# Kernel optimization log

Measured on AMD Instinct MI355X. Metric: run time of the kernel, lower is better.

The kernel has to match this reference:

```python
import jax, jax.numpy as jnp
import numpy as np

N_QUBITS = 4
N_LAYERS = 3
INV_SQRT2 = 0.7071067811865476
BSZ = 262144


def _apply_ry(state, wire, theta):
    # state: [B,2,2,2,2] complex; theta: [B] (per-batch rotation angle)
    s = jnp.moveaxis(state, wire + 1, -1)
    a0, a1 = s[..., 0], s[..., 1]
    c = jnp.cos(theta * 0.5)[:, None, None, None]
    sn = jnp.sin(theta * 0.5)[:, None, None, None]
    out = jnp.stack([c * a0 - sn * a1, sn * a0 + c * a1], axis=-1)
    return jnp.moveaxis(out, -1, wire + 1)


def _apply_h(state, wire):
    s = jnp.moveaxis(state, wire + 1, -1)
    a0, a1 = s[..., 0], s[..., 1]
    out = jnp.stack([(a0 + a1) * INV_SQRT2, (a0 - a1) * INV_SQRT2], axis=-1)
    return jnp.moveaxis(out, -1, wire + 1)


def _apply_crz(state, cw, tw, phi):
    # controlled-RZ: phase exp(-/+ i*phi/2) on |c=1,t=0/1>; phi is a scalar param
    s = jnp.moveaxis(state, (cw + 1, tw + 1), (-2, -1))
    phase = jnp.exp(1j * phi * jnp.array([-0.5, 0.5], dtype=jnp.float32)).astype(s.dtype)
    s = s.at[..., 1, :].multiply(phase)
    return jnp.moveaxis(s, (-2, -1), (cw + 1, tw + 1))


def _circuit(angles, weights):
    # angles: [B,4]; weights: [12]; returns PauliZ expvals [B,4]
    B = angles.shape[0]
    state = jnp.zeros((B, 2, 2, 2, 2), jnp.complex64).at[:, 0, 0, 0, 0].set(1.0)
    for i in range(N_QUBITS):
        state = _apply_ry(state, i, angles[:, i])
    for l in range(N_LAYERS):
        lp = weights[N_QUBITS * l: N_QUBITS * (l + 1)]
        for i in range(N_QUBITS):
            state = _apply_crz(state, i, (i + 1) % N_QUBITS, lp[i])
        for i in range(N_QUBITS):
            state = _apply_h(state, i)
    p = state.real ** 2 + state.imag ** 2  # [B,2,2,2,2] probabilities
    z = jnp.stack(
        [jnp.take(p, 0, axis=w + 1).sum(axis=(1, 2, 3))
         - jnp.take(p, 1, axis=w + 1).sum(axis=(1, 2, 3))
         for w in range(N_QUBITS)],
        axis=-1,
    )
    return z


def setup_inputs() -> dict:
    key = jax.random.key(0)
    k1, k2, k3, k4 = jax.random.split(key, 4)
    x = jax.random.uniform(k1, (BSZ, 16), dtype=jnp.float32)
    weights = jax.random.normal(k2, (N_LAYERS * N_QUBITS,), dtype=jnp.float32)
    lin_w = jax.random.normal(k3, (2, 16), dtype=jnp.float32) * 0.25
    lin_b = jax.random.normal(k4, (2,), dtype=jnp.float32) * 0.1
    return {"x": x, "weights": weights, "lin_w": lin_w, "lin_b": lin_b}


def reference(x, weights, lin_w, lin_b):
    bsz = x.shape[0]
    # 4x4 image -> four 2x2 patches in loop order (0,0),(0,2),(2,0),(2,2);
    # each patch flattened row-major: [x[j,k], x[j,k+1], x[j+1,k], x[j+1,k+1]]
    xv = x.reshape(bsz, 2, 2, 2, 2).transpose(0, 1, 3, 2, 4).reshape(bsz * 4, 4)
    q = _circuit(xv, weights).reshape(bsz, 16)  # patch-major feature order as in torch cat
    logits = q @ lin_w.T + lin_b
    return jax.nn.softmax(logits, axis=1)
```

## Files before the change

### kernel.cpp

```cpp
#include <hip/hip_runtime.h>


__device__ __forceinline__ float layer_angle(const float* __restrict__ w,
                                             int l, int idx) {
    float ang = 0.f;
    #pragma unroll
    for (int g = 0; g < 4; ++g) {
        int cb = (idx >> (3 - g)) & 1;
        int tb = (idx >> (3 - ((g + 1) & 3))) & 1;
        if (cb) ang += (tb ? 0.5f : -0.5f) * w[l * 4 + g];
    }
    return ang;
}

__global__ __launch_bounds__(256) void precompute_tensors(
    const float* __restrict__ weights,
    const float* __restrict__ lin_w,
    const float* __restrict__ lin_b,
    float* __restrict__ ws)
{
    __shared__ float2 U1[256], U2[256], U[256];
    __shared__ float zeta[4][16];
    __shared__ float G[4][256];
    __shared__ float A[4][3][64];
    __shared__ float B[4][9][16];
    __shared__ float C1[4][27][4];
    int t = threadIdx.x;
    int i = t >> 4, j = t & 15;

    {
        float sgn = (__popc(i & j) & 1) ? -1.f : 1.f;
        float a = layer_angle(weights, 0, j);
        U1[t] = make_float2(sgn * __cosf(a), sgn * __sinf(a));
    }
    if (t < 64) {
        int s = t >> 4, k = t & 15;
        float z = 0.f;
        #pragma unroll
        for (int w = 0; w < 4; ++w) {
            float sg = ((k >> (3 - w)) & 1) ? -1.f : 1.f;
            z += (lin_w[s * 4 + w] - lin_w[16 + s * 4 + w]) * sg;
        }
        zeta[s][k] = z;
    }
    __syncthreads();
    {
        float ar = 0.f, ai = 0.f;
        for (int k = 0; k < 16; ++k) {
            float sgn = (__popc(i & k) & 1) ? -1.f : 1.f;
            float a = layer_angle(weights, 1, k);
            float cr = sgn * __cosf(a), ci = sgn * __sinf(a);
            float2 u = U1[k * 16 + j];
            ar += cr * u.x - ci * u.y;
            ai += cr * u.y + ci * u.x;
        }
        U2[t] = make_float2(ar, ai);
    }
    __syncthreads();
    {
        float ar = 0.f, ai = 0.f;
        for (int k = 0; k < 16; ++k) {
            float sgn = (__popc(i & k) & 1) ? -1.f : 1.f;
            float a = layer_angle(weights, 2, k);
            float cr = sgn * __cosf(a), ci = sgn * __sinf(a);
            float2 u = U2[k * 16 + j];
            ar += cr * u.x - ci * u.y;
            ai += cr * u.y + ci * u.x;
        }
        U[t] = make_float2(ar, ai);
    }
    __syncthreads();
    {
        float g[4] = {0, 0, 0, 0};
        for (int k = 0; k < 16; ++k) {
            float2 uki = U[k * 16 + i], ukj = U[k * 16 + j];
            float p = uki.x * ukj.x + uki.y * ukj.y;
            #pragma unroll
            for (int s = 0; s < 4; ++s) g[s] += zeta[s][k] * p;
        }
        #pragma unroll
        for (int s = 0; s < 4; ++s) G[s][t] = g[s];
    }
    __syncthreads();
    for (int e = t; e < 768; e += 256) {
        int m = e / 192, r = e % 192;
        int t3 = r / 64, q = r % 64;
        int ih = q >> 3, jh = q & 7;
        float g00 = G[m][(ih * 2 + 0) * 16 + jh * 2 + 0];
        float g01 = G[m][(ih * 2 + 0) * 16 + jh * 2 + 1];
        float g10 = G[m][(ih * 2 + 1) * 16 + jh * 2 + 0];
        float g11 = G[m][(ih * 2 + 1) * 16 + jh * 2 + 1];
        A[m][t3][q] = (t3 == 0) ? g00 + g11 : (t3 == 1) ? g00 - g11 : g01 + g10;
    }
    __syncthreads();
    for (int e = t; e < 576; e += 256) {
        int m = e / 144, r = e % 144;
        int t2 = r / 48; r %= 48;
        int t3 = r / 16, q = r % 16;
        int ih = q >> 2, jh = q & 3;
        float a00 = A[m][t3][(ih * 2 + 0) * 8 + jh * 2 + 0];
        float a01 = A[m][t3][(ih * 2 + 0) * 8 + jh * 2 + 1];
        float a10 = A[m][t3][(ih * 2 + 1) * 8 + jh * 2 + 0];
        float a11 = A[m][t3][(ih * 2 + 1) * 8 + jh * 2 + 1];
        B[m][t2 * 3 + t3][q] = (t2 == 0) ? a00 + a11
                             : (t2 == 1) ? a00 - a11 : a01 + a10;
    }
    __syncthreads();
    for (int e = t; e < 432; e += 256) {
        int m = e / 108, r = e % 108;
        int t1 = r / 36; r %= 36;
        int t23 = r / 4, q = r % 4;
        int ih = q >> 1, jh = q & 1;
        float b00 = B[m][t23][(ih * 2 + 0) * 4 + jh * 2 + 0];
        float b01 = B[m][t23][(ih * 2 + 0) * 4 + jh * 2 + 1];
        float b10 = B[m][t23][(ih * 2 + 1) * 4 + jh * 2 + 0];
        float b11 = B[m][t23][(ih * 2 + 1) * 4 + jh * 2 + 1];
        C1[m][t1 * 9 + t23][q] = (t1 == 0) ? b00 + b11
                               : (t1 == 1) ? b00 - b11 : b01 + b10;
    }
    __syncthreads();
    {
        const float scale = 1.f / 65536.f;
        float bias = lin_b[0] - lin_b[1];
        for (int e = t; e < 324; e += 256) {
            int m = e / 81, r = e % 81;
            int t0 = r / 27, t123 = r % 27;
            const float* c = C1[m][t123];
            float v = (t0 == 0) ? c[0] + c[3] : (t0 == 1) ? c[0] - c[3]
                                              : c[1] + c[2];
            float val = v * scale;
            if (e == 0) val += bias;
            int t1 = t123 / 9, k = t123 % 9;
            ws[(m * 9 + t0 * 3 + t1) * 12 + k] = val;
        }
    }
}

__global__ __launch_bounds__(256) void qcircuit_kernel(
    const float* __restrict__ x,
    const float* __restrict__ tab,
    float* __restrict__ out,
    int nrows)
{
    __shared__ __align__(16) float tabs[4][9][12];

    int t = threadIdx.x;
    if (t < 108) ((float4*)tabs)[t] = ((const float4*)tab)[t];

    int b = blockIdx.x * blockDim.x + t;
    int bc = b < nrows ? b : 0;
    const float4* xp = (const float4*)(x + (size_t)bc * 16);
    float4 xa = xp[0], xb = xp[1], xc = xp[2], xd = xp[3];
    float xs[16] = {xa.x, xa.y, xa.z, xa.w, xb.x, xb.y, xb.z, xb.w,
                    xc.x, xc.y, xc.z, xc.w, xd.x, xd.y, xd.z, xd.w};
    __syncthreads();

    float d = 0.f;
    #pragma unroll
    for (int s = 0; s < 4; ++s) {
        const int b0 = ((s >> 1) << 3) + ((s & 1) << 1);
        float C0, S0, C1v, S1, C2, S2, C3, S3;
        __sincosf(xs[b0],     &S0,  &C0);
        __sincosf(xs[b0 + 1], &S1,  &C1v);
        __sincosf(xs[b0 + 4], &S2,  &C2);
        __sincosf(xs[b0 + 5], &S3,  &C3);
        #pragma unroll
        for (int t0 = 0; t0 < 3; ++t0) {
            float acc = 0.f;
            #pragma unroll
            for (int t1 = 0; t1 < 3; ++t1) {
                const float* tp = &tabs[s][t0 * 3 + t1][0];
                float4 q0 = *(const float4*)tp;
                float4 q1 = *(const float4*)(tp + 4);
                float  k8 = tp[8];
                float u0 = fmaf(S3, q0.z, fmaf(C3, q0.y, q0.x));
                float u1 = fmaf(S3, q1.y, fmaf(C3, q1.x, q0.w));
                float u2 = fmaf(S3, k8,   fmaf(C3, q1.w, q1.z));
                float a1 = fmaf(S2, u2, fmaf(C2, u1, u0));
                acc = (t1 == 0) ? acc + a1
                    : (t1 == 1) ? fmaf(C1v, a1, acc)
                                : fmaf(S1,  a1, acc);
            }
            d = (t0 == 0) ? d + acc
              : (t0 == 1) ? fmaf(C0, acc, d)
                          : fmaf(S0, acc, d);
        }
    }

    if (b < nrows) {
        float p0 = 1.f / (1.f + __expf(-d));
        *(float2*)(out + (size_t)b * 2) = make_float2(p0, 1.f - p0);
    }
}

extern "C" void kernel_launch(void* const* d_in, const int* in_sizes, int n_in,
                              void* d_out, int out_size, void* d_ws, size_t ws_size,
                              hipStream_t stream) {
    const float* x       = (const float*)d_in[0];
    const float* weights = (const float*)d_in[1];
    const float* lin_w   = (const float*)d_in[2];
    const float* lin_b   = (const float*)d_in[3];
    float* out = (float*)d_out;
    float* ws  = (float*)d_ws;

    int nrows = in_sizes[0] / 16;

    precompute_tensors<<<1, 256, 0, stream>>>(weights, lin_w, lin_b, ws);

    int block = 256;
    int grid = (nrows + block - 1) / block;
    qcircuit_kernel<<<grid, block, 0, stream>>>(x, ws, out, nrows);
}
```

Baseline: 76.46 us.

## Fuse table precompute into main kernel, recomputing tables per 1024-thread block

Merges the single-block precompute kernel and the per-row evaluation kernel into one launch. Each 1024-thread block now redundantly rebuilds the contracted circuit tables in shared memory from the weights, with the x loads issued up front to overlap. This removes a serial kernel launch and the workspace round trip. In exchange, every block (256 of them) repeats the 16x16 complex matrix products, and the larger block plus larger shared footprint may lower occupancy.

```diff
diff --git a/kernel.cpp b/kernel.cpp
--- a/kernel.cpp
+++ b/kernel.cpp
@@ -13,11 +13,13 @@
     return ang;
 }
 
-__global__ __launch_bounds__(256) void precompute_tensors(
+__global__ __launch_bounds__(1024) void fused_qcircuit(
+    const float* __restrict__ x,
     const float* __restrict__ weights,
     const float* __restrict__ lin_w,
     const float* __restrict__ lin_b,
-    float* __restrict__ ws)
+    float* __restrict__ out,
+    int nrows)
 {
     __shared__ float2 U1[256], U2[256], U[256];
     __shared__ float zeta[4][16];
@@ -25,10 +27,17 @@
     __shared__ float A[4][3][64];
     __shared__ float B[4][9][16];
     __shared__ float C1[4][27][4];
+    __shared__ __align__(16) float tabs[4][9][12];
+
     int t = threadIdx.x;
     int i = t >> 4, j = t & 15;
 
-    {
+    int b = blockIdx.x * blockDim.x + t;
+    int bc = b < nrows ? b : 0;
+    const float4* xp = (const float4*)(x + (size_t)bc * 16);
+    float4 xa = xp[0], xb = xp[1], xc = xp[2], xd = xp[3];
+
+    if (t < 256) {
         float sgn = (__popc(i & j) & 1) ? -1.f : 1.f;
         float a = layer_angle(weights, 0, j);
         U1[t] = make_float2(sgn * __cosf(a), sgn * __sinf(a));
@@ -44,7 +53,7 @@
         zeta[s][k] = z;
     }
     __syncthreads();
-    {
+    if (t < 256) {
         float ar = 0.f, ai = 0.f;
         for (int k = 0; k < 16; ++k) {
             float sgn = (__popc(i & k) & 1) ? -1.f : 1.f;
@@ -57,7 +66,7 @@
         U2[t] = make_float2(ar, ai);
     }
     __syncthreads();
-    {
+    if (t < 256) {
         float ar = 0.f, ai = 0.f;
         for (int k = 0; k < 16; ++k) {
             float sgn = (__popc(i & k) & 1) ? -1.f : 1.f;
@@ -70,7 +79,7 @@
         U[t] = make_float2(ar, ai);
     }
     __syncthreads();
-    {
+    if (t < 256) {
         float g[4] = {0, 0, 0, 0};
         for (int k = 0; k < 16; ++k) {
             float2 uki = U[k * 16 + i], ukj = U[k * 16 + j];
@@ -82,7 +91,7 @@
         for (int s = 0; s < 4; ++s) G[s][t] = g[s];
     }
     __syncthreads();
-    for (int e = t; e < 768; e += 256) {
+    for (int e = t; e < 768; e += 1024) {
         int m = e / 192, r = e % 192;
         int t3 = r / 64, q = r % 64;
         int ih = q >> 3, jh = q & 7;
@@ -93,7 +102,7 @@
         A[m][t3][q] = (t3 == 0) ? g00 + g11 : (t3 == 1) ? g00 - g11 : g01 + g10;
     }
     __syncthreads();
-    for (int e = t; e < 576; e += 256) {
+    for (int e = t; e < 576; e += 1024) {
         int m = e / 144, r = e % 144;
         int t2 = r / 48; r %= 48;
         int t3 = r / 16, q = r % 16;
@@ -106,7 +115,7 @@
                              : (t2 == 1) ? a00 - a11 : a01 + a10;
     }
     __syncthreads();
-    for (int e = t; e < 432; e += 256) {
+    for (int e = t; e < 432; e += 1024) {
         int m = e / 108, r = e % 108;
         int t1 = r / 36; r %= 36;
         int t23 = r / 4, q = r % 4;
@@ -122,7 +131,7 @@
     {
         const float scale = 1.f / 65536.f;
         float bias = lin_b[0] - lin_b[1];
-        for (int e = t; e < 324; e += 256) {
+        for (int e = t; e < 324; e += 1024) {
             int m = e / 81, r = e % 81;
             int t0 = r / 27, t123 = r % 27;
             const float* c = C1[m][t123];
@@ -131,30 +140,13 @@
             float val = v * scale;
             if (e == 0) val += bias;
             int t1 = t123 / 9, k = t123 % 9;
-            ws[(m * 9 + t0 * 3 + t1) * 12 + k] = val;
-        }
-    }
-}
-
-__global__ __launch_bounds__(256) void qcircuit_kernel(
-    const float* __restrict__ x,
-    const float* __restrict__ tab,
-    float* __restrict__ out,
-    int nrows)
-{
-    __shared__ __align__(16) float tabs[4][9][12];
-
-    int t = threadIdx.x;
-    if (t < 108) ((float4*)tabs)[t] = ((const float4*)tab)[t];
-
-    int b = blockIdx.x * blockDim.x + t;
-    int bc = b < nrows ? b : 0;
-    const float4* xp = (const float4*)(x + (size_t)bc * 16);
-    float4 xa = xp[0], xb = xp[1], xc = xp[2], xd = xp[3];
+            tabs[m][t0 * 3 + t1][k] = val;
+        }
+    }
+    __syncthreads();
+
     float xs[16] = {xa.x, xa.y, xa.z, xa.w, xb.x, xb.y, xb.z, xb.w,
                     xc.x, xc.y, xc.z, xc.w, xd.x, xd.y, xd.z, xd.w};
-    __syncthreads();
-
     float d = 0.f;
     #pragma unroll
     for (int s = 0; s < 4; ++s) {
@@ -191,6 +183,47 @@
         float p0 = 1.f / (1.f + __expf(-d));
         *(float2*)(out + (size_t)b * 2) = make_float2(p0, 1.f - p0);
     }
+
+    for (int row = b + gridDim.x * blockDim.x; row < nrows;
+         row += gridDim.x * blockDim.x) {
+        const float4* xq = (const float4*)(x + (size_t)row * 16);
+        float4 ya = xq[0], yb = xq[1], yc = xq[2], yd = xq[3];
+        float ys[16] = {ya.x, ya.y, ya.z, ya.w, yb.x, yb.y, yb.z, yb.w,
+                        yc.x, yc.y, yc.z, yc.w, yd.x, yd.y, yd.z, yd.w};
+        float dd = 0.f;
+        #pragma unroll
+        for (int s = 0; s < 4; ++s) {
+            const int b0 = ((s >> 1) << 3) + ((s & 1) << 1);
+            float C0, S0, C1v, S1, C2, S2, C3, S3;
+            __sincosf(ys[b0],     &S0,  &C0);
+            __sincosf(ys[b0 + 1], &S1,  &C1v);
+            __sincosf(ys[b0 + 4], &S2,  &C2);
+            __sincosf(ys[b0 + 5], &S3,  &C3);
+            #pragma unroll
+            for (int t0 = 0; t0 < 3; ++t0) {
+                float acc = 0.f;
+                #pragma unroll
+                for (int t1 = 0; t1 < 3; ++t1) {
+                    const float* tp = &tabs[s][t0 * 3 + t1][0];
+                    float4 q0 = *(const float4*)tp;
+                    float4 q1 = *(const float4*)(tp + 4);
+                    float  k8 = tp[8];
+                    float u0 = fmaf(S3, q0.z, fmaf(C3, q0.y, q0.x));
+                    float u1 = fmaf(S3, q1.y, fmaf(C3, q1.x, q0.w));
+                    float u2 = fmaf(S3, k8,   fmaf(C3, q1.w, q1.z));
+                    float a1 = fmaf(S2, u2, fmaf(C2, u1, u0));
+                    acc = (t1 == 0) ? acc + a1
+                        : (t1 == 1) ? fmaf(C1v, a1, acc)
+                                    : fmaf(S1,  a1, acc);
+                }
+                dd = (t0 == 0) ? dd + acc
+                   : (t0 == 1) ? fmaf(C0, acc, dd)
+                               : fmaf(S0, acc, dd);
+            }
+        }
+        float p0 = 1.f / (1.f + __expf(-dd));
+        *(float2*)(out + (size_t)row * 2) = make_float2(p0, 1.f - p0);
+    }
 }
 
 extern "C" void kernel_launch(void* const* d_in, const int* in_sizes, int n_in,
@@ -201,13 +234,10 @@
     const float* lin_w   = (const float*)d_in[2];
     const float* lin_b   = (const float*)d_in[3];
     float* out = (float*)d_out;
-    float* ws  = (float*)d_ws;
 
     int nrows = in_sizes[0] / 16;
-
-    precompute_tensors<<<1, 256, 0, stream>>>(weights, lin_w, lin_b, ws);
-
-    int block = 256;
+    int block = 1024;
     int grid = (nrows + block - 1) / block;
-    qcircuit_kernel<<<grid, block, 0, stream>>>(x, ws, out, nrows);
+    if (grid < 1) grid = 1;
+    fused_qcircuit<<<grid, block, 0, stream>>>(x, weights, lin_w, lin_b, out, nrows);
 }
```

Measured after the change: 73.78 us, median of 2. -3.5%, faster.
